# Optimization experiments

Measured on AMD Instinct MI355X. Metric: run time of the kernel, lower is better.

The kernel has to match this reference:

```python
import jax, jax.numpy as jnp
import numpy as np

PAD = 0
SIGMA_C = 2.0
EPS = 1e-6
LOG_SQRT_2PI = 0.9189385332046727  # log(sqrt(2*pi))

B, T_CHAR, VOCAB, D_EMB = 32, 256, 100, 384


def setup_inputs() -> dict:
    rng = np.random.default_rng(0)
    # text tokens in [1, VOCAB): avoid pad (=0) inside the utterance
    text = rng.integers(1, VOCAB, size=(B, T_CHAR), dtype=np.int64)
    # per-char durations in frames, 1..8
    durs = rng.integers(1, 9, size=(B, T_CHAR), dtype=np.int32)
    # total_time = length of repeat_interleave(text, durs) padded to batch max
    total_time = int(durs.sum(axis=-1).max())
    key = jax.random.key(0)
    embed = jax.random.normal(key, (VOCAB, D_EMB), dtype=jnp.float32)
    return {
        "text": jnp.asarray(text),
        "durs": jnp.asarray(durs),
        "embed": embed,
        "total_time": total_time,
    }


def reference(text, durs, embed, total_time):
    # Pad 2 trailing positions: pad token, zero duration (as in the original)
    text = jnp.pad(text, ((0, 0), (0, 2)), constant_values=PAD)      # [B, Tc]
    durs = jnp.pad(durs, ((0, 0), (0, 2)), constant_values=0)        # [B, Tc]
    durs_f = durs.astype(jnp.float32)

    # Gaussian centers: mid-point of each char's frame span
    csum = jnp.cumsum(durs_f, axis=-1)
    c = durs_f / 2.0 + jnp.pad(csum[:, :-1], ((0, 0), (1, 0)))       # [B, Tc]
    sig = durs_f / SIGMA_C + EPS                                     # [B, Tc]

    t = jnp.arange(total_time, dtype=jnp.float32) + 0.5              # [Tt]

    # Gaussian pdf evaluated at frame times: w[b, t, c]
    z = (t[None, :, None] - c[:, None, :]) / sig[:, None, :]         # [B, Tt, Tc]
    w = jnp.exp(-0.5 * z * z - jnp.log(sig)[:, None, :] - LOG_SQRT_2PI)

    # zero padded-char columns, normalize over chars
    char_pad = (text == PAD)[:, None, :]                             # [B, 1, Tc]
    w = jnp.where(char_pad, 0.0, w)
    w = w / (jnp.sum(w, axis=-1, keepdims=True) + EPS)

    # time positions past each utterance's total duration are padding:
    # zero the whole row, then put weight 1.0 on the last (pad) char column
    total_dur = jnp.sum(durs, axis=-1)                               # [B]
    time_pad = jnp.arange(total_time)[None, :] >= total_dur[:, None] # [B, Tt]
    w = jnp.where(time_pad[:, :, None], 0.0, w)
    w = w.at[:, :, -1].set(jnp.where(time_pad, 1.0, w[:, :, -1]))

    # aggregate gathered embeddings: [B, Tt, Tc] x [B, Tc, D] -> [B, Tt, D]
    u = jnp.einsum("btc,bcd->btd", w, embed[text])
    return u
```

## Files before the change

kernel.cpp:

```cpp
#include <hip/hip_runtime.h>

#define TC 256
#define DEMB 384
#define VOC 100
#define WIN 96
#define TTILE 32
#define WPS 104
#define CST 288
#define LOG_SQRT_2PI 0.9189385332046727f

typedef short v8s __attribute__((ext_vector_type(8)));
typedef float v4f __attribute__((ext_vector_type(4)));

__device__ __forceinline__ unsigned short f32_to_bf16_rne(float f) {
    union { float f; unsigned int u; } x; x.f = f;
    unsigned int u = x.u;
    return (unsigned short)((u + 0x7FFFu + ((u >> 16) & 1u)) >> 16);
}

__global__ __launch_bounds__(256) void gather_transpose_kernel(
    const int* __restrict__ text, const float* __restrict__ embed,
    unsigned short* __restrict__ ET)
{
    int i = blockIdx.x * 256 + threadIdx.x;
    int c = i % CST;
    int r = i / CST;
    int nseg = r & 3;
    int b = r >> 2;
    if (c >= TC || b >= 32) return;
    int v = text[b * TC + c];
    const float* erow = embed + (size_t)v * DEMB + nseg * 96;
    unsigned short* dst = ET + ((size_t)b * DEMB + nseg * 96) * CST + c;
#pragma unroll
    for (int k = 0; k < 24; ++k) {
        float4 e = *(const float4*)(erow + 4 * k);
        dst[(4 * k + 0) * CST] = f32_to_bf16_rne(e.x);
        dst[(4 * k + 1) * CST] = f32_to_bf16_rne(e.y);
        dst[(4 * k + 2) * CST] = f32_to_bf16_rne(e.z);
        dst[(4 * k + 3) * CST] = f32_to_bf16_rne(e.w);
    }
}

__global__ __launch_bounds__(256, 4) void gauss_embed_mfma_kernel(
    const int* __restrict__ text,
    const int* __restrict__ durs,
    const float* __restrict__ embed,
    const unsigned short* __restrict__ ET,
    float* __restrict__ out,
    int Tt)
{
    const int b   = blockIdx.y;
    const int t0  = blockIdx.x * TTILE;
    const int tid = threadIdx.x;
    const int wv   = tid >> 6;
    const int lane = tid & 63;
    const int nq   = lane & 15;
    const int q    = lane >> 4;

    __shared__ float s_scan[TC];
    __shared__ float s_part[256];
    __shared__ __align__(16) unsigned short s_wp[TTILE * WPS];
    __shared__ float s_invS[TTILE];
    __shared__ int   s_j0, s_totdur;

    s_scan[tid] = (float)durs[b * TC + tid];
    if (tid == 0) s_j0 = TC - 1;
    __syncthreads();
    for (int ofs = 1; ofs < TC; ofs <<= 1) {
        float v = (tid >= ofs) ? s_scan[tid - ofs] : 0.0f;
        __syncthreads();
        s_scan[tid] += v;
        __syncthreads();
    }

    {
        int en = (int)s_scan[tid];
        int st = tid ? (int)s_scan[tid - 1] : 0;
        if (t0 >= st && t0 < en) s_j0 = tid;
        if (tid == 0) s_totdur = (int)s_scan[TC - 1];
    }
    __syncthreads();

    int base = s_j0 - 31;
    base = base < 0 ? 0 : base;
    base &= ~7;
    base = base > TC - WIN ? TC - WIN : base;
    const int totdur = s_totdur;

    {
        const int t = tid & 31;
        const int g = tid >> 5;
        const float tf = (float)(t0 + t) + 0.5f;
        float lsum = 0.0f;
#pragma unroll
        for (int cc = 0; cc < 12; ++cc) {
            int c = g * 12 + cc;
            int j = base + c;
            float endf   = s_scan[j];
            float startf = j ? s_scan[j - 1] : 0.0f;
            float dur = endf - startf;
            float sig = dur * 0.5f + 1e-6f;
            float ctr = endf - dur * 0.5f;
            float z = (tf - ctr) / sig;
            float w = __expf(fmaf(-0.5f * z, z, -__logf(sig) - LOG_SQRT_2PI));
            lsum += w;
            s_wp[t * WPS + c] = f32_to_bf16_rne(w);
        }
        s_part[tid] = lsum;
    }
    __syncthreads();

    if (tid < TTILE) {
        float s = 1e-6f;
#pragma unroll
        for (int g = 0; g < 8; ++g) s += s_part[g * 32 + tid];
        s_invS[tid] = 1.0f / s;
    }
    __syncthreads();

    const unsigned short* ETb = ET + (size_t)b * DEMB * CST;

    v4f acc[6][2];
#pragma unroll
    for (int nt = 0; nt < 6; ++nt)
#pragma unroll
        for (int mt = 0; mt < 2; ++mt) {
            v4f z = {0.0f, 0.0f, 0.0f, 0.0f};
            acc[nt][mt] = z;
        }

#pragma unroll
    for (int ks = 0; ks < 3; ++ks) {
        const int c0 = ks * 32 + q * 8;
        v8s a0 = *(const v8s*)(s_wp + nq * WPS + c0);
        v8s a1 = *(const v8s*)(s_wp + (16 + nq) * WPS + c0);
#pragma unroll
        for (int nt = 0; nt < 6; ++nt) {
            v8s bf = *(const v8s*)(ETb + (size_t)(wv * 96 + nt * 16 + nq) * CST + base + c0);
            acc[nt][0] = __builtin_amdgcn_mfma_f32_16x16x32_bf16(a0, bf, acc[nt][0], 0, 0, 0);
            acc[nt][1] = __builtin_amdgcn_mfma_f32_16x16x32_bf16(a1, bf, acc[nt][1], 0, 0, 0);
        }
    }

    float pe[6];
#pragma unroll
    for (int nt = 0; nt < 6; ++nt) pe[nt] = embed[wv * 96 + nt * 16 + nq];

#pragma unroll
    for (int mt = 0; mt < 2; ++mt) {
#pragma unroll
        for (int r = 0; r < 4; ++r) {
            int tl = mt * 16 + q * 4 + r;
            int t = t0 + tl;
            if (t >= Tt) continue;
            float sv = s_invS[tl];
            bool pad = (t >= totdur);
            float* orow = out + (size_t)(b * Tt + t) * DEMB + wv * 96 + nq;
#pragma unroll
            for (int nt = 0; nt < 6; ++nt) {
                float val = pad ? pe[nt] : acc[nt][mt][r] * sv;
                orow[nt * 16] = val;
            }
        }
    }
}

extern "C" void kernel_launch(void* const* d_in, const int* in_sizes, int n_in,
                              void* d_out, int out_size, void* d_ws, size_t ws_size,
                              hipStream_t stream) {
    const int*   text  = (const int*)d_in[0];
    const int*   durs  = (const int*)d_in[1];
    const float* embed = (const float*)d_in[2];
    float* out = (float*)d_out;

    const int B = 32;
    const int Tt = out_size / (B * DEMB);

    unsigned short* ET = (unsigned short*)d_ws;
    {
        int nthreads = 32 * 4 * CST;
        gather_transpose_kernel<<<(nthreads + 255) / 256, 256, 0, stream>>>(text, embed, ET);
    }

    dim3 grid((Tt + TTILE - 1) / TTILE, B);
    gauss_embed_mfma_kernel<<<grid, 256, 0, stream>>>(text, durs, embed, ET, out, Tt);
}
```

Measured before the change: 101.2 us.

## Hoist duration scan into prep kernel and fast-path fully padded tiles

Moves the per-batch duration prefix scan, the Gaussian centres, inverse sigmas and log terms, and the per-tile window start into the prep kernel, which now also performs the embedding gather and transpose with finer-grained threads. The main kernel no longer runs a barrier-heavy scan in every block. Tiles lying entirely past the utterance length now just copy the pad embedding row and skip the MFMA work. The costs are extra workspace arrays, a dependency on fixed workspace offsets, and a j0A table that only covers up to 64 tiles per batch.

After: 100.5 us. Within noise of the previous version (-0.7%).

```diff
diff --git a/kernel.cpp b/kernel.cpp
--- a/kernel.cpp
+++ b/kernel.cpp
@@ -18,74 +18,109 @@
     return (unsigned short)((u + 0x7FFFu + ((u >> 16) & 1u)) >> 16);
 }
 
-__global__ __launch_bounds__(256) void gather_transpose_kernel(
-    const int* __restrict__ text, const float* __restrict__ embed,
-    unsigned short* __restrict__ ET)
+__global__ __launch_bounds__(256) void prep_kernel(
+    const int* __restrict__ text, const int* __restrict__ durs,
+    const float* __restrict__ embed,
+    unsigned short* __restrict__ ET,
+    float* __restrict__ ctrA, float* __restrict__ isgA, float* __restrict__ lgA,
+    int* __restrict__ j0A, int* __restrict__ totA)
 {
-    int i = blockIdx.x * 256 + threadIdx.x;
-    int c = i % CST;
-    int r = i / CST;
-    int nseg = r & 3;
-    int b = r >> 2;
-    if (c >= TC || b >= 32) return;
-    int v = text[b * TC + c];
-    const float* erow = embed + (size_t)v * DEMB + nseg * 96;
-    unsigned short* dst = ET + ((size_t)b * DEMB + nseg * 96) * CST + c;
-#pragma unroll
-    for (int k = 0; k < 24; ++k) {
-        float4 e = *(const float4*)(erow + 4 * k);
-        dst[(4 * k + 0) * CST] = f32_to_bf16_rne(e.x);
-        dst[(4 * k + 1) * CST] = f32_to_bf16_rne(e.y);
-        dst[(4 * k + 2) * CST] = f32_to_bf16_rne(e.z);
-        dst[(4 * k + 3) * CST] = f32_to_bf16_rne(e.w);
-    }
-}
-
-__global__ __launch_bounds__(256, 4) void gauss_embed_mfma_kernel(
-    const int* __restrict__ text,
-    const int* __restrict__ durs,
+    if (blockIdx.x < 576) {
+        int i = blockIdx.x * 256 + threadIdx.x;
+        int c = i % CST;
+        int r = i / CST;
+        int nseg = r & 15;
+        int b = r >> 4;
+        if (c >= TC) return;
+        int v = text[b * TC + c];
+        const float* erow = embed + (size_t)v * DEMB + nseg * 24;
+        unsigned short* dst = ET + ((size_t)b * DEMB + nseg * 24) * CST + c;
+#pragma unroll
+        for (int k = 0; k < 6; ++k) {
+            float4 e = *(const float4*)(erow + 4 * k);
+            dst[(4 * k + 0) * CST] = f32_to_bf16_rne(e.x);
+            dst[(4 * k + 1) * CST] = f32_to_bf16_rne(e.y);
+            dst[(4 * k + 2) * CST] = f32_to_bf16_rne(e.z);
+            dst[(4 * k + 3) * CST] = f32_to_bf16_rne(e.w);
+        }
+    } else {
+        const int b = blockIdx.x - 576;
+        const int c = threadIdx.x;
+        const int lane = c & 63, wv = c >> 6;
+        int d = durs[b * TC + c];
+        int x = d;
+#pragma unroll
+        for (int ofs = 1; ofs < 64; ofs <<= 1) {
+            int n = __shfl_up(x, ofs, 64);
+            if (lane >= ofs) x += n;
+        }
+        __shared__ int s_wsum[4];
+        if (lane == 63) s_wsum[wv] = x;
+        __syncthreads();
+        int pre = 0;
+        for (int k = 0; k < wv; ++k) pre += s_wsum[k];
+        int en = pre + x;
+        int st = en - d;
+        if (c == TC - 1) totA[b] = en;
+
+        float df  = (float)d;
+        float sig = df * 0.5f + 1e-6f;
+        ctrA[b * TC + c] = (float)st + df * 0.5f;
+        isgA[b * TC + c] = 1.0f / sig;
+        lgA[b * TC + c]  = -logf(sig) - LOG_SQRT_2PI;
+
+        for (int t0 = ((st + 31) >> 5) << 5; t0 < en; t0 += 32)
+            j0A[b * 64 + (t0 >> 5)] = c;
+    }
+}
+
+__global__ __launch_bounds__(256, 2) void gauss_embed_mfma_kernel(
     const float* __restrict__ embed,
     const unsigned short* __restrict__ ET,
-    float* __restrict__ out,
-    int Tt)
+    const float* __restrict__ ctrA, const float* __restrict__ isgA,
+    const float* __restrict__ lgA,
+    const int* __restrict__ j0A, const int* __restrict__ totA,
+    float* __restrict__ out, int Tt)
 {
     const int b   = blockIdx.y;
     const int t0  = blockIdx.x * TTILE;
     const int tid = threadIdx.x;
+    const int totdur = totA[b];
+
+    if (t0 >= totdur) {
+        const float4* e0 = (const float4*)embed;
+        int row = tid >> 3, q4 = tid & 7;
+        int t = t0 + row;
+        if (t < Tt) {
+            float4* orow = (float4*)(out + (size_t)(b * Tt + t) * DEMB);
+#pragma unroll
+            for (int k = 0; k < 12; ++k) orow[q4 + 8 * k] = e0[q4 + 8 * k];
+        }
+        return;
+    }
+
     const int wv   = tid >> 6;
     const int lane = tid & 63;
     const int nq   = lane & 15;
     const int q    = lane >> 4;
 
-    __shared__ float s_scan[TC];
+    __shared__ float s_ctr[WIN], s_isg[WIN], s_A[WIN];
+    __shared__ __align__(16) unsigned short s_wp[TTILE * WPS];
     __shared__ float s_part[256];
-    __shared__ __align__(16) unsigned short s_wp[TTILE * WPS];
     __shared__ float s_invS[TTILE];
-    __shared__ int   s_j0, s_totdur;
-
-    s_scan[tid] = (float)durs[b * TC + tid];
-    if (tid == 0) s_j0 = TC - 1;
-    __syncthreads();
-    for (int ofs = 1; ofs < TC; ofs <<= 1) {
-        float v = (tid >= ofs) ? s_scan[tid - ofs] : 0.0f;
-        __syncthreads();
-        s_scan[tid] += v;
-        __syncthreads();
-    }
-
-    {
-        int en = (int)s_scan[tid];
-        int st = tid ? (int)s_scan[tid - 1] : 0;
-        if (t0 >= st && t0 < en) s_j0 = tid;
-        if (tid == 0) s_totdur = (int)s_scan[TC - 1];
-    }
-    __syncthreads();
-
-    int base = s_j0 - 31;
+
+    int j0 = j0A[b * 64 + (t0 >> 5)];
+    int base = j0 - 31;
     base = base < 0 ? 0 : base;
     base &= ~7;
-    base = base > TC - WIN ? TC - WIN : base;
-    const int totdur = s_totdur;
+    if (base > TC - WIN) base = TC - WIN;
+
+    if (tid < WIN) {
+        s_ctr[tid] = ctrA[b * TC + base + tid];
+        s_isg[tid] = isgA[b * TC + base + tid];
+        s_A[tid]   = lgA[b * TC + base + tid];
+    }
+    __syncthreads();
 
     {
         const int t = tid & 31;
@@ -95,14 +130,8 @@
 #pragma unroll
         for (int cc = 0; cc < 12; ++cc) {
             int c = g * 12 + cc;
-            int j = base + c;
-            float endf   = s_scan[j];
-            float startf = j ? s_scan[j - 1] : 0.0f;
-            float dur = endf - startf;
-            float sig = dur * 0.5f + 1e-6f;
-            float ctr = endf - dur * 0.5f;
-            float z = (tf - ctr) / sig;
-            float w = __expf(fmaf(-0.5f * z, z, -__logf(sig) - LOG_SQRT_2PI));
+            float z = (tf - s_ctr[c]) * s_isg[c];
+            float w = __expf(fmaf(-0.5f * z, z, s_A[c]));
             lsum += w;
             s_wp[t * WPS + c] = f32_to_bf16_rne(w);
         }
@@ -118,7 +147,7 @@
     }
     __syncthreads();
 
-    const unsigned short* ETb = ET + (size_t)b * DEMB * CST;
+    const unsigned short* ETb = ET + (size_t)b * DEMB * CST + base;
 
     v4f acc[6][2];
 #pragma unroll
@@ -136,15 +165,18 @@
         v8s a1 = *(const v8s*)(s_wp + (16 + nq) * WPS + c0);
 #pragma unroll
         for (int nt = 0; nt < 6; ++nt) {
-            v8s bf = *(const v8s*)(ETb + (size_t)(wv * 96 + nt * 16 + nq) * CST + base + c0);
+            v8s bf = *(const v8s*)(ETb + (size_t)(wv * 96 + nt * 16 + nq) * CST + c0);
             acc[nt][0] = __builtin_amdgcn_mfma_f32_16x16x32_bf16(a0, bf, acc[nt][0], 0, 0, 0);
             acc[nt][1] = __builtin_amdgcn_mfma_f32_16x16x32_bf16(a1, bf, acc[nt][1], 0, 0, 0);
         }
     }
 
+    const bool anypad = (t0 + TTILE > totdur);
     float pe[6];
-#pragma unroll
-    for (int nt = 0; nt < 6; ++nt) pe[nt] = embed[wv * 96 + nt * 16 + nq];
+    if (anypad) {
+#pragma unroll
+        for (int nt = 0; nt < 6; ++nt) pe[nt] = embed[wv * 96 + nt * 16 + nq];
+    }
 
 #pragma unroll
     for (int mt = 0; mt < 2; ++mt) {
@@ -154,7 +186,7 @@
             int t = t0 + tl;
             if (t >= Tt) continue;
             float sv = s_invS[tl];
-            bool pad = (t >= totdur);
+            bool pad = anypad && (t >= totdur);
             float* orow = out + (size_t)(b * Tt + t) * DEMB + wv * 96 + nq;
 #pragma unroll
             for (int nt = 0; nt < 6; ++nt) {
@@ -176,12 +208,18 @@
     const int B = 32;
     const int Tt = out_size / (B * DEMB);
 
-    unsigned short* ET = (unsigned short*)d_ws;
-    {
-        int nthreads = 32 * 4 * CST;
-        gather_transpose_kernel<<<(nthreads + 255) / 256, 256, 0, stream>>>(text, embed, ET);
-    }
+    char* ws = (char*)d_ws;
+    unsigned short* ET = (unsigned short*)ws;
+    float* ctrA = (float*)(ws + 7077888);
+    float* isgA = (float*)(ws + 7077888 + 32768);
+    float* lgA  = (float*)(ws + 7077888 + 65536);
+    int*   j0A  = (int*)  (ws + 7077888 + 98304);
+    int*   totA = (int*)  (ws + 7077888 + 106496);
+
+    prep_kernel<<<608, 256, 0, stream>>>(text, durs, embed, ET,
+                                         ctrA, isgA, lgA, j0A, totA);
 
     dim3 grid((Tt + TTILE - 1) / TTILE, B);
-    gauss_embed_mfma_kernel<<<grid, 256, 0, stream>>>(text, durs, embed, ET, out, Tt);
-}
+    gauss_embed_mfma_kernel<<<grid, 256, 0, stream>>>(embed, ET, ctrA, isgA, lgA,
+                                                      j0A, totA, out, Tt);
+}
```
